# Performance work log

Hardware: AMD Instinct MI355X
Metric: run time of the kernel (lower is better)

The kernel has to match this reference:

```python
import jax, jax.numpy as jnp
import numpy as np


def setup_inputs() -> dict:
    key = jax.random.key(0)
    k1, k2, k3, k4 = jax.random.split(key, 4)
    B, S, D, R = 32, 512, 1024, 256
    batch = jax.random.normal(k1, (B, S, D), dtype=jnp.float32)
    # params initialized uniform(-0.05, 0.05) in the original
    proj_L = jax.random.uniform(k2, (D, R), minval=-0.05, maxval=0.05, dtype=jnp.float32)
    proj_R = jax.random.uniform(k3, (R, D), minval=-0.05, maxval=0.05, dtype=jnp.float32)
    bias = jax.random.uniform(k4, (1,), minval=-0.05, maxval=0.05, dtype=jnp.float32)
    return {"batch": batch, "proj_L": proj_L, "proj_R": proj_R, "bias": bias}


def reference(batch, proj_L, proj_R, bias):
    # logits[b,i,j] = batch[b,i] @ (L @ R) @ batch[b,j] + bias
    # Computed as (batch @ L) @ (batch @ R^T)^T -- two batched GEMMs,
    # avoiding the O(B*S^2*D) expanded intermediate of the original.
    # Dropout is identity in eval mode.
    left = jnp.einsum('bsd,dr->bsr', batch, proj_L)   # [B,S,R]
    right = jnp.einsum('rd,btd->brt', proj_R, batch)  # [B,R,S]
    logits = jnp.einsum('bsr,brt->bst', left, right) + bias[0]
    return logits
```

## Files before the change

### kernel.cpp

```cpp
#include <hip/hip_runtime.h>
#include <hip/hip_bf16.h>
#include <stdint.h>

typedef __attribute__((ext_vector_type(8))) __bf16 bf16x8;
typedef __attribute__((ext_vector_type(4))) float f32x4;

static constexpr int Bb = 32, Ss = 512, Dd = 1024, Rr = 256;

__device__ __forceinline__ void gload_lds16(const void* g, void* l) {
  __builtin_amdgcn_global_load_lds(
      (const __attribute__((address_space(1))) void*)g,
      (__attribute__((address_space(3))) void*)l, 16, 0, 0);
}

__global__ __launch_bounds__(256) void prep_kernel(
    const float* __restrict__ L, const float* __restrict__ R,
    __bf16* __restrict__ Bt) {
  int i = blockIdx.x * 256 + threadIdx.x;
  int n = i >> 10;
  int d = i & (Dd - 1);
  float v = (n < Rr) ? L[d * Rr + n] : R[(size_t)(n - Rr) * Dd + d];
  Bt[i] = (__bf16)v;
}

__global__ __launch_bounds__(256, 4) void proj_gemm(
    const float* __restrict__ batch,
    const __bf16* __restrict__ Bt,
    __bf16* __restrict__ outL,
    __bf16* __restrict__ outR) {
  const int s = (blockIdx.x & 7) * 128 + (blockIdx.x >> 3);
  const int mt = s >> 2;
  const int nt = s & 3;
  const int m0 = mt * 64, n0 = nt * 128;

  __shared__ __align__(16) char smem[32768];

  const int t = threadIdx.x;
  const int lane = t & 63;
  const int wave = t >> 6;
  const int wr = wave >> 1, wc = wave & 1;

  f32x4 acc[2][4] = {};

  for (int it = 0; it < 16; ++it) {
    const int k0 = it * 64;
    __syncthreads();
#pragma unroll
    for (int q = 0; q < 4; ++q) {
      int e = q * 256 + t;
      int row = e >> 4, g = e & 15;
      int gsrc = g ^ (row & 7);
      gload_lds16(batch + (size_t)(m0 + row) * Dd + k0 + gsrc * 4,
                  smem + e * 16);
    }
#pragma unroll
    for (int q = 0; q < 4; ++q) {
      int e = q * 256 + t;
      int row = e >> 3, g = e & 7;
      int gsrc = g ^ (row & 7);
      gload_lds16(Bt + (size_t)(n0 + row) * Dd + k0 + gsrc * 8,
                  smem + 16384 + e * 16);
    }
    __syncthreads();

#pragma unroll
    for (int kk = 0; kk < 2; ++kk) {
      bf16x8 a[2], b[4];
#pragma unroll
      for (int m = 0; m < 2; ++m) {
        int row = wr * 32 + m * 16 + (lane & 15);
        int ga = kk * 8 + (lane >> 4) * 2;
        f32x4 v0 = *(const f32x4*)(smem + row * 256 + ((ga ^ (row & 7))) * 16);
        f32x4 v1 =
            *(const f32x4*)(smem + row * 256 + (((ga + 1) ^ (row & 7))) * 16);
        bf16x8 av;
        av[0] = (__bf16)v0[0]; av[1] = (__bf16)v0[1];
        av[2] = (__bf16)v0[2]; av[3] = (__bf16)v0[3];
        av[4] = (__bf16)v1[0]; av[5] = (__bf16)v1[1];
        av[6] = (__bf16)v1[2]; av[7] = (__bf16)v1[3];
        a[m] = av;
      }
#pragma unroll
      for (int n = 0; n < 4; ++n) {
        int row = wc * 64 + n * 16 + (lane & 15);
        int g = kk * 4 + (lane >> 4);
        b[n] = *(const bf16x8*)(smem + 16384 +
                                (row * 8 + (g ^ (row & 7))) * 16);
      }
#pragma unroll
      for (int m = 0; m < 2; ++m)
#pragma unroll
        for (int n = 0; n < 4; ++n)
          acc[m][n] = __builtin_amdgcn_mfma_f32_16x16x32_bf16(a[m], b[n],
                                                              acc[m][n], 0, 0, 0);
    }
  }

  __bf16* out = (n0 < Rr) ? outL : outR;
  const int cb = n0 & (Rr - 1);
  const int col = lane & 15, rgrp = lane >> 4;
#pragma unroll
  for (int m = 0; m < 2; ++m) {
    int r0 = m0 + wr * 32 + m * 16 + rgrp * 4;
#pragma unroll
    for (int n = 0; n < 4; ++n) {
      int c = cb + wc * 64 + n * 16 + col;
#pragma unroll
      for (int i = 0; i < 4; ++i)
        out[(size_t)(r0 + i) * Rr + c] = (__bf16)acc[m][n][i];
    }
  }
}

__global__ __launch_bounds__(256, 4) void score_gemm(
    const __bf16* __restrict__ left,
    const __bf16* __restrict__ right,
    const float* __restrict__ biasp,
    float* __restrict__ out) {
  const int nt = blockIdx.x;
  const int mt = blockIdx.y;
  const int bz = blockIdx.z;
  const __bf16* A = left + (size_t)bz * Ss * Rr;
  const __bf16* B = right + (size_t)bz * Ss * Rr;
  float* O = out + (size_t)bz * Ss * Ss;
  const int m0 = mt * 64, n0 = nt * 128;

  __shared__ __align__(16) char smem[24576];

  const int t = threadIdx.x;
  const int lane = t & 63;
  const int wave = t >> 6;
  const int wr = wave >> 1, wc = wave & 1;

  f32x4 acc[2][4] = {};

  for (int it = 0; it < 4; ++it) {
    const int k0 = it * 64;
    __syncthreads();
#pragma unroll
    for (int q = 0; q < 2; ++q) {
      int e = q * 256 + t;
      int row = e >> 3, g = e & 7;
      int gsrc = g ^ (row & 7);
      gload_lds16(A + (size_t)(m0 + row) * Rr + k0 + gsrc * 8, smem + e * 16);
    }
#pragma unroll
    for (int q = 0; q < 4; ++q) {
      int e = q * 256 + t;
      int row = e >> 3, g = e & 7;
      int gsrc = g ^ (row & 7);
      gload_lds16(B + (size_t)(n0 + row) * Rr + k0 + gsrc * 8,
                  smem + 8192 + e * 16);
    }
    __syncthreads();

#pragma unroll
    for (int kk = 0; kk < 2; ++kk) {
      bf16x8 a[2], b[4];
#pragma unroll
      for (int m = 0; m < 2; ++m) {
        int row = wr * 32 + m * 16 + (lane & 15);
        int g = kk * 4 + (lane >> 4);
        a[m] = *(const bf16x8*)(smem + (row * 8 + (g ^ (row & 7))) * 16);
      }
#pragma unroll
      for (int n = 0; n < 4; ++n) {
        int row = wc * 64 + n * 16 + (lane & 15);
        int g = kk * 4 + (lane >> 4);
        b[n] = *(const bf16x8*)(smem + 8192 +
                                (row * 8 + (g ^ (row & 7))) * 16);
      }
#pragma unroll
      for (int m = 0; m < 2; ++m)
#pragma unroll
        for (int n = 0; n < 4; ++n)
          acc[m][n] = __builtin_amdgcn_mfma_f32_16x16x32_bf16(a[m], b[n],
                                                              acc[m][n], 0, 0, 0);
    }
  }

  const float bias = *biasp;
  const int col = lane & 15, rgrp = lane >> 4;
#pragma unroll
  for (int m = 0; m < 2; ++m) {
    int r0 = m0 + wr * 32 + m * 16 + rgrp * 4;
#pragma unroll
    for (int n = 0; n < 4; ++n) {
      int c = n0 + wc * 64 + n * 16 + col;
#pragma unroll
      for (int i = 0; i < 4; ++i)
        O[(size_t)(r0 + i) * Ss + c] = acc[m][n][i] + bias;
    }
  }
}

extern "C" void kernel_launch(void* const* d_in, const int* in_sizes, int n_in,
                              void* d_out, int out_size, void* d_ws,
                              size_t ws_size, hipStream_t stream) {
  const float* batch = (const float*)d_in[0];
  const float* projL = (const float*)d_in[1];
  const float* projR = (const float*)d_in[2];
  const float* bias = (const float*)d_in[3];
  float* out = (float*)d_out;

  char* ws = (char*)d_ws;
  __bf16* left = (__bf16*)(ws);
  __bf16* right = (__bf16*)(ws + 8388608);
  __bf16* Btc = (__bf16*)(ws + 16777216);

  prep_kernel<<<dim3(2048), dim3(256), 0, stream>>>(projL, projR, Btc);
  proj_gemm<<<dim3(1024), dim3(256), 0, stream>>>(batch, Btc, left, right);
  score_gemm<<<dim3(4, 8, 32), dim3(256), 0, stream>>>(left, right, bias, out);
}
```

Measured before the change: 52.02 us.

## Rework projection GEMM with larger tiles and double-buffered register-staged prefetch

```diff
diff --git a/kernel.cpp b/kernel.cpp
--- a/kernel.cpp
+++ b/kernel.cpp
@@ -23,88 +23,103 @@
   Bt[i] = (__bf16)v;
 }
 
-__global__ __launch_bounds__(256, 4) void proj_gemm(
+__global__ __launch_bounds__(512, 2) void proj_gemm(
     const float* __restrict__ batch,
     const __bf16* __restrict__ Bt,
     __bf16* __restrict__ outL,
     __bf16* __restrict__ outR) {
-  const int s = (blockIdx.x & 7) * 128 + (blockIdx.x >> 3);
-  const int mt = s >> 2;
-  const int nt = s & 3;
-  const int m0 = mt * 64, n0 = nt * 128;
-
-  __shared__ __align__(16) char smem[32768];
+  const int s = (blockIdx.x & 7) * 32 + (blockIdx.x >> 3);
+  const int mt = s >> 1;
+  const int nt = s & 1;
+  const int m0 = mt * 128, n0 = nt * 256;
+
+  __shared__ __align__(16) char smem[49152];
 
   const int t = threadIdx.x;
   const int lane = t & 63;
   const int wave = t >> 6;
-  const int wr = wave >> 1, wc = wave & 1;
-
-  f32x4 acc[2][4] = {};
-
-  for (int it = 0; it < 16; ++it) {
-    const int k0 = it * 64;
-    __syncthreads();
-#pragma unroll
-    for (int q = 0; q < 4; ++q) {
-      int e = q * 256 + t;
-      int row = e >> 4, g = e & 15;
-      int gsrc = g ^ (row & 7);
-      gload_lds16(batch + (size_t)(m0 + row) * Dd + k0 + gsrc * 4,
-                  smem + e * 16);
-    }
-#pragma unroll
-    for (int q = 0; q < 4; ++q) {
-      int e = q * 256 + t;
-      int row = e >> 3, g = e & 7;
-      int gsrc = g ^ (row & 7);
-      gload_lds16(Bt + (size_t)(n0 + row) * Dd + k0 + gsrc * 8,
-                  smem + 16384 + e * 16);
-    }
-    __syncthreads();
-
-#pragma unroll
-    for (int kk = 0; kk < 2; ++kk) {
-      bf16x8 a[2], b[4];
-#pragma unroll
-      for (int m = 0; m < 2; ++m) {
-        int row = wr * 32 + m * 16 + (lane & 15);
-        int ga = kk * 8 + (lane >> 4) * 2;
-        f32x4 v0 = *(const f32x4*)(smem + row * 256 + ((ga ^ (row & 7))) * 16);
-        f32x4 v1 =
-            *(const f32x4*)(smem + row * 256 + (((ga + 1) ^ (row & 7))) * 16);
-        bf16x8 av;
-        av[0] = (__bf16)v0[0]; av[1] = (__bf16)v0[1];
-        av[2] = (__bf16)v0[2]; av[3] = (__bf16)v0[3];
-        av[4] = (__bf16)v1[0]; av[5] = (__bf16)v1[1];
-        av[6] = (__bf16)v1[2]; av[7] = (__bf16)v1[3];
-        a[m] = av;
-      }
-#pragma unroll
-      for (int n = 0; n < 4; ++n) {
-        int row = wc * 64 + n * 16 + (lane & 15);
-        int g = kk * 4 + (lane >> 4);
-        b[n] = *(const bf16x8*)(smem + 16384 +
-                                (row * 8 + (g ^ (row & 7))) * 16);
-      }
-#pragma unroll
-      for (int m = 0; m < 2; ++m)
-#pragma unroll
-        for (int n = 0; n < 4; ++n)
-          acc[m][n] = __builtin_amdgcn_mfma_f32_16x16x32_bf16(a[m], b[n],
-                                                              acc[m][n], 0, 0, 0);
-    }
-  }
-
-  __bf16* out = (n0 < Rr) ? outL : outR;
-  const int cb = n0 & (Rr - 1);
+  const int wr = wave >> 2, wc = wave & 3;
+
+  f32x4 acc[4][4] = {};
+  f32x4 areg0, areg1;
+
+  const int arow = t >> 2, ag = t & 3;
+  const int ags = ag ^ ((arow >> 1) & 3);
+
+  auto issueA = [&](int k0) {
+    const float* src = batch + (size_t)(m0 + arow) * Dd + k0 + ag * 8;
+    areg0 = *(const f32x4*)src;
+    areg1 = *(const f32x4*)(src + 4);
+  };
+  auto writeA = [&](int buf) {
+    bf16x8 v;
+    v[0] = (__bf16)areg0[0]; v[1] = (__bf16)areg0[1];
+    v[2] = (__bf16)areg0[2]; v[3] = (__bf16)areg0[3];
+    v[4] = (__bf16)areg1[0]; v[5] = (__bf16)areg1[1];
+    v[6] = (__bf16)areg1[2]; v[7] = (__bf16)areg1[3];
+    *(bf16x8*)(smem + buf * 8192 + (arow * 4 + ags) * 16) = v;
+  };
+  auto stageB = [&](int buf, int k0) {
+#pragma unroll
+    for (int p = 0; p < 2; ++p) {
+      int e = p * 512 + t;
+      int row = e >> 2, g = e & 3;
+      int gs = g ^ ((row >> 1) & 3);
+      gload_lds16(Bt + (size_t)(n0 + row) * Dd + k0 + gs * 8,
+                  smem + 16384 + buf * 16384 + e * 16);
+    }
+  };
+  auto compute = [&](int buf) {
+    const char* Ab = smem + buf * 8192;
+    const char* Bb = smem + 16384 + buf * 16384;
+    bf16x8 a[4], b[4];
+    const int g = lane >> 4;
+#pragma unroll
+    for (int m = 0; m < 4; ++m) {
+      int row = wr * 64 + m * 16 + (lane & 15);
+      a[m] = *(const bf16x8*)(Ab + (row * 4 + (g ^ ((row >> 1) & 3))) * 16);
+    }
+#pragma unroll
+    for (int n = 0; n < 4; ++n) {
+      int row = wc * 64 + n * 16 + (lane & 15);
+      b[n] = *(const bf16x8*)(Bb + (row * 4 + (g ^ ((row >> 1) & 3))) * 16);
+    }
+#pragma unroll
+    for (int m = 0; m < 4; ++m)
+#pragma unroll
+      for (int n = 0; n < 4; ++n)
+        acc[m][n] = __builtin_amdgcn_mfma_f32_16x16x32_bf16(a[m], b[n],
+                                                            acc[m][n], 0, 0, 0);
+  };
+
+  issueA(0);
+  stageB(0, 0);
+  writeA(0);
+  int cur = 0;
+  for (int it = 0; it < 32; ++it) {
+    if (it < 31) {
+      issueA(it * 32 + 32);
+      stageB(cur ^ 1, it * 32 + 32);
+      asm volatile("s_waitcnt vmcnt(4)" ::: "memory");
+    } else {
+      asm volatile("s_waitcnt vmcnt(0)" ::: "memory");
+    }
+    __builtin_amdgcn_s_barrier();
+    compute(cur);
+    if (it < 31) writeA(cur ^ 1);
+    asm volatile("s_waitcnt lgkmcnt(0)" ::: "memory");
+    __builtin_amdgcn_s_barrier();
+    cur ^= 1;
+  }
+
+  __bf16* out = nt ? outR : outL;
   const int col = lane & 15, rgrp = lane >> 4;
 #pragma unroll
-  for (int m = 0; m < 2; ++m) {
-    int r0 = m0 + wr * 32 + m * 16 + rgrp * 4;
+  for (int m = 0; m < 4; ++m) {
+    int r0 = m0 + wr * 64 + m * 16 + rgrp * 4;
 #pragma unroll
     for (int n = 0; n < 4; ++n) {
-      int c = cb + wc * 64 + n * 16 + col;
+      int c = wc * 64 + n * 16 + col;
 #pragma unroll
       for (int i = 0; i < 4; ++i)
         out[(size_t)(r0 + i) * Rr + c] = (__bf16)acc[m][n][i];
@@ -209,6 +224,6 @@
   __bf16* Btc = (__bf16*)(ws + 16777216);
 
   prep_kernel<<<dim3(2048), dim3(256), 0, stream>>>(projL, projR, Btc);
-  proj_gemm<<<dim3(1024), dim3(256), 0, stream>>>(batch, Btc, left, right);
+  proj_gemm<<<dim3(256), dim3(512), 0, stream>>>(batch, Btc, left, right);
   score_gemm<<<dim3(4, 8, 32), dim3(256), 0, stream>>>(left, right, bias, out);
 }
```

Measured after the change: 54.28 us. +4.3%, slower.

## Double-buffer proj_gemm and convert batch tile to bf16 once in registers

Applied to the files above, without the earlier changes.

```diff
diff --git a/kernel.cpp b/kernel.cpp
--- a/kernel.cpp
+++ b/kernel.cpp
@@ -23,17 +23,17 @@
   Bt[i] = (__bf16)v;
 }
 
-__global__ __launch_bounds__(256, 4) void proj_gemm(
+__global__ __launch_bounds__(256, 3) void proj_gemm(
     const float* __restrict__ batch,
     const __bf16* __restrict__ Bt,
     __bf16* __restrict__ outL,
     __bf16* __restrict__ outR) {
-  const int s = (blockIdx.x & 7) * 128 + (blockIdx.x >> 3);
+  const int s = ((blockIdx.x & 7) << 7) + (blockIdx.x >> 3);
   const int mt = s >> 2;
   const int nt = s & 3;
   const int m0 = mt * 64, n0 = nt * 128;
 
-  __shared__ __align__(16) char smem[32768];
+  __shared__ __align__(16) char smem[49152];
 
   const int t = threadIdx.x;
   const int lane = t & 63;
@@ -41,51 +41,59 @@
   const int wr = wave >> 1, wc = wave & 1;
 
   f32x4 acc[2][4] = {};
-
-  for (int it = 0; it < 16; ++it) {
-    const int k0 = it * 64;
-    __syncthreads();
-#pragma unroll
-    for (int q = 0; q < 4; ++q) {
-      int e = q * 256 + t;
-      int row = e >> 4, g = e & 15;
-      int gsrc = g ^ (row & 7);
-      gload_lds16(batch + (size_t)(m0 + row) * Dd + k0 + gsrc * 4,
-                  smem + e * 16);
-    }
-#pragma unroll
-    for (int q = 0; q < 4; ++q) {
-      int e = q * 256 + t;
+  f32x4 areg[4];
+
+  const int arow = t >> 2, ag = t & 3;
+  const int ags = ag ^ (arow & 7);
+
+  auto issueA = [&](int k0) {
+    const float* src = batch + (size_t)(m0 + arow) * Dd + k0 + ag * 8;
+    areg[0] = *(const f32x4*)src;
+    areg[1] = *(const f32x4*)(src + 4);
+    areg[2] = *(const f32x4*)(src + 32);
+    areg[3] = *(const f32x4*)(src + 36);
+  };
+  auto writeA = [&](int buf) {
+    char* Ab = smem + buf * 8192;
+    bf16x8 v0, v1;
+    v0[0] = (__bf16)areg[0][0]; v0[1] = (__bf16)areg[0][1];
+    v0[2] = (__bf16)areg[0][2]; v0[3] = (__bf16)areg[0][3];
+    v0[4] = (__bf16)areg[1][0]; v0[5] = (__bf16)areg[1][1];
+    v0[6] = (__bf16)areg[1][2]; v0[7] = (__bf16)areg[1][3];
+    v1[0] = (__bf16)areg[2][0]; v1[1] = (__bf16)areg[2][1];
+    v1[2] = (__bf16)areg[2][2]; v1[3] = (__bf16)areg[2][3];
+    v1[4] = (__bf16)areg[3][0]; v1[5] = (__bf16)areg[3][1];
+    v1[6] = (__bf16)areg[3][2]; v1[7] = (__bf16)areg[3][3];
+    *(bf16x8*)(Ab + (arow * 8 + ags) * 16) = v0;
+    *(bf16x8*)(Ab + (arow * 8 + (ags ^ 4)) * 16) = v1;
+  };
+  auto stageB = [&](int buf, int k0) {
+    char* Bbuf = smem + 16384 + buf * 16384;
+#pragma unroll
+    for (int p = 0; p < 4; ++p) {
+      int e = p * 256 + t;
       int row = e >> 3, g = e & 7;
-      int gsrc = g ^ (row & 7);
-      gload_lds16(Bt + (size_t)(n0 + row) * Dd + k0 + gsrc * 8,
-                  smem + 16384 + e * 16);
-    }
-    __syncthreads();
-
+      int gs = g ^ (row & 7);
+      gload_lds16(Bt + (size_t)(n0 + row) * Dd + k0 + gs * 8,
+                  Bbuf + e * 16);
+    }
+  };
+  auto compute = [&](int buf) {
+    const char* Ab = smem + buf * 8192;
+    const char* Bbuf = smem + 16384 + buf * 16384;
 #pragma unroll
     for (int kk = 0; kk < 2; ++kk) {
+      const int g = kk * 4 + (lane >> 4);
       bf16x8 a[2], b[4];
 #pragma unroll
       for (int m = 0; m < 2; ++m) {
         int row = wr * 32 + m * 16 + (lane & 15);
-        int ga = kk * 8 + (lane >> 4) * 2;
-        f32x4 v0 = *(const f32x4*)(smem + row * 256 + ((ga ^ (row & 7))) * 16);
-        f32x4 v1 =
-            *(const f32x4*)(smem + row * 256 + (((ga + 1) ^ (row & 7))) * 16);
-        bf16x8 av;
-        av[0] = (__bf16)v0[0]; av[1] = (__bf16)v0[1];
-        av[2] = (__bf16)v0[2]; av[3] = (__bf16)v0[3];
-        av[4] = (__bf16)v1[0]; av[5] = (__bf16)v1[1];
-        av[6] = (__bf16)v1[2]; av[7] = (__bf16)v1[3];
-        a[m] = av;
+        a[m] = *(const bf16x8*)(Ab + (row * 8 + (g ^ (row & 7))) * 16);
       }
 #pragma unroll
       for (int n = 0; n < 4; ++n) {
         int row = wc * 64 + n * 16 + (lane & 15);
-        int g = kk * 4 + (lane >> 4);
-        b[n] = *(const bf16x8*)(smem + 16384 +
-                                (row * 8 + (g ^ (row & 7))) * 16);
+        b[n] = *(const bf16x8*)(Bbuf + (row * 8 + (g ^ (row & 7))) * 16);
       }
 #pragma unroll
       for (int m = 0; m < 2; ++m)
@@ -94,6 +102,23 @@
           acc[m][n] = __builtin_amdgcn_mfma_f32_16x16x32_bf16(a[m], b[n],
                                                               acc[m][n], 0, 0, 0);
     }
+  };
+
+  issueA(0);
+  stageB(0, 0);
+  writeA(0);
+  __syncthreads();
+
+#pragma unroll 1
+  for (int tt = 0; tt < 16; ++tt) {
+    const int buf = tt & 1;
+    if (tt < 15) {
+      issueA(tt * 64 + 64);
+      stageB(buf ^ 1, tt * 64 + 64);
+    }
+    compute(buf);
+    if (tt < 15) writeA(buf ^ 1);
+    __syncthreads();
   }
 
   __bf16* out = (n0 < Rr) ? outL : outR;
```

Result: slower. 54.05 us (+3.9%).

## Restructure projection GEMM: direct-register A loads, double-buffered B, 32x32 MFMA

Applied to the files above, without the earlier changes.

```diff
diff --git a/kernel.cpp b/kernel.cpp
--- a/kernel.cpp
+++ b/kernel.cpp
@@ -4,6 +4,7 @@
 
 typedef __attribute__((ext_vector_type(8))) __bf16 bf16x8;
 typedef __attribute__((ext_vector_type(4))) float f32x4;
+typedef __attribute__((ext_vector_type(16))) float f32x16;
 
 static constexpr int Bb = 32, Ss = 512, Dd = 1024, Rr = 256;
 
@@ -23,93 +24,123 @@
   Bt[i] = (__bf16)v;
 }
 
-__global__ __launch_bounds__(256, 4) void proj_gemm(
+__global__ __launch_bounds__(256, 3) void proj_gemm(
     const float* __restrict__ batch,
     const __bf16* __restrict__ Bt,
     __bf16* __restrict__ outL,
     __bf16* __restrict__ outR) {
-  const int s = (blockIdx.x & 7) * 128 + (blockIdx.x >> 3);
+  const int s = ((blockIdx.x & 7) << 6) + (blockIdx.x >> 3);
   const int mt = s >> 2;
   const int nt = s & 3;
-  const int m0 = mt * 64, n0 = nt * 128;
-
-  __shared__ __align__(16) char smem[32768];
+  const int m0 = mt * 128, n0 = nt * 128;
+
+  __shared__ __align__(16) char smem[16384];
 
   const int t = threadIdx.x;
   const int lane = t & 63;
   const int wave = t >> 6;
   const int wr = wave >> 1, wc = wave & 1;
 
-  f32x4 acc[2][4] = {};
-
-  for (int it = 0; it < 16; ++it) {
-    const int k0 = it * 64;
+  f32x16 acc[2][2] = {};
+
+  const float* abase =
+      batch + (size_t)(m0 + wr * 64 + (lane & 31)) * Dd + (lane >> 5) * 8;
+
+  f32x4 anext[8];
+  bf16x8 acur[4];
+
+  auto loadAraw = [&](int k0) {
+#pragma unroll
+    for (int mi = 0; mi < 2; ++mi)
+#pragma unroll
+      for (int ks = 0; ks < 2; ++ks) {
+        const float* p = abase + (size_t)mi * 32 * Dd + k0 + ks * 16;
+        anext[(mi * 2 + ks) * 2] = *(const f32x4*)p;
+        anext[(mi * 2 + ks) * 2 + 1] = *(const f32x4*)(p + 4);
+      }
+  };
+  auto cvtA = [&]() {
+#pragma unroll
+    for (int q = 0; q < 4; ++q) {
+      f32x4 lo = anext[2 * q], hi = anext[2 * q + 1];
+      bf16x8 v;
+      v[0] = (__bf16)lo[0]; v[1] = (__bf16)lo[1];
+      v[2] = (__bf16)lo[2]; v[3] = (__bf16)lo[3];
+      v[4] = (__bf16)hi[0]; v[5] = (__bf16)hi[1];
+      v[6] = (__bf16)hi[2]; v[7] = (__bf16)hi[3];
+      acur[q] = v;
+    }
+  };
+  auto stageB = [&](int buf, int k0) {
+    char* Bbuf = smem + buf * 8192;
+#pragma unroll
+    for (int p = 0; p < 2; ++p) {
+      int e = p * 256 + t;
+      int row = e >> 2, g = e & 3;
+      int gs = g ^ (row & 3);
+      gload_lds16(Bt + (size_t)(n0 + row) * Dd + k0 + gs * 8, Bbuf + e * 16);
+    }
+  };
+
+  loadAraw(0);
+  stageB(0, 0);
+  cvtA();
+  __syncthreads();
+
+#pragma unroll 1
+  for (int tt = 0; tt < 32; ++tt) {
+    const int buf = tt & 1;
+    const char* Bbuf = smem + buf * 8192;
+    if (tt < 31) stageB(buf ^ 1, tt * 32 + 32);
+
+    bf16x8 b0[2], b1[2];
+#pragma unroll
+    for (int ni = 0; ni < 2; ++ni) {
+      int row = wc * 64 + ni * 32 + (lane & 31);
+      int kg = 0 * 2 + (lane >> 5);
+      b0[ni] = *(const bf16x8*)(Bbuf + (row * 4 + (kg ^ (row & 3))) * 16);
+    }
+#pragma unroll
+    for (int mi = 0; mi < 2; ++mi)
+#pragma unroll
+      for (int ni = 0; ni < 2; ++ni)
+        acc[mi][ni] = __builtin_amdgcn_mfma_f32_32x32x16_bf16(
+            acur[mi * 2 + 0], b0[ni], acc[mi][ni], 0, 0, 0);
+
+    if (tt < 31) loadAraw(tt * 32 + 32);
+
+#pragma unroll
+    for (int ni = 0; ni < 2; ++ni) {
+      int row = wc * 64 + ni * 32 + (lane & 31);
+      int kg = 1 * 2 + (lane >> 5);
+      b1[ni] = *(const bf16x8*)(Bbuf + (row * 4 + (kg ^ (row & 3))) * 16);
+    }
+#pragma unroll
+    for (int mi = 0; mi < 2; ++mi)
+#pragma unroll
+      for (int ni = 0; ni < 2; ++ni)
+        acc[mi][ni] = __builtin_amdgcn_mfma_f32_32x32x16_bf16(
+            acur[mi * 2 + 1], b1[ni], acc[mi][ni], 0, 0, 0);
+
     __syncthreads();
-#pragma unroll
-    for (int q = 0; q < 4; ++q) {
-      int e = q * 256 + t;
-      int row = e >> 4, g = e & 15;
-      int gsrc = g ^ (row & 7);
-      gload_lds16(batch + (size_t)(m0 + row) * Dd + k0 + gsrc * 4,
-                  smem + e * 16);
-    }
-#pragma unroll
-    for (int q = 0; q < 4; ++q) {
-      int e = q * 256 + t;
-      int row = e >> 3, g = e & 7;
-      int gsrc = g ^ (row & 7);
-      gload_lds16(Bt + (size_t)(n0 + row) * Dd + k0 + gsrc * 8,
-                  smem + 16384 + e * 16);
-    }
-    __syncthreads();
-
-#pragma unroll
-    for (int kk = 0; kk < 2; ++kk) {
-      bf16x8 a[2], b[4];
-#pragma unroll
-      for (int m = 0; m < 2; ++m) {
-        int row = wr * 32 + m * 16 + (lane & 15);
-        int ga = kk * 8 + (lane >> 4) * 2;
-        f32x4 v0 = *(const f32x4*)(smem + row * 256 + ((ga ^ (row & 7))) * 16);
-        f32x4 v1 =
-            *(const f32x4*)(smem + row * 256 + (((ga + 1) ^ (row & 7))) * 16);
-        bf16x8 av;
-        av[0] = (__bf16)v0[0]; av[1] = (__bf16)v0[1];
-        av[2] = (__bf16)v0[2]; av[3] = (__bf16)v0[3];
-        av[4] = (__bf16)v1[0]; av[5] = (__bf16)v1[1];
-        av[6] = (__bf16)v1[2]; av[7] = (__bf16)v1[3];
-        a[m] = av;
-      }
-#pragma unroll
-      for (int n = 0; n < 4; ++n) {
-        int row = wc * 64 + n * 16 + (lane & 15);
-        int g = kk * 4 + (lane >> 4);
-        b[n] = *(const bf16x8*)(smem + 16384 +
-                                (row * 8 + (g ^ (row & 7))) * 16);
-      }
-#pragma unroll
-      for (int m = 0; m < 2; ++m)
-#pragma unroll
-        for (int n = 0; n < 4; ++n)
-          acc[m][n] = __builtin_amdgcn_mfma_f32_16x16x32_bf16(a[m], b[n],
-                                                              acc[m][n], 0, 0, 0);
-    }
+    if (tt < 31) cvtA();
   }
 
   __bf16* out = (n0 < Rr) ? outL : outR;
   const int cb = n0 & (Rr - 1);
-  const int col = lane & 15, rgrp = lane >> 4;
-#pragma unroll
-  for (int m = 0; m < 2; ++m) {
-    int r0 = m0 + wr * 32 + m * 16 + rgrp * 4;
-#pragma unroll
-    for (int n = 0; n < 4; ++n) {
-      int c = cb + wc * 64 + n * 16 + col;
-#pragma unroll
-      for (int i = 0; i < 4; ++i)
-        out[(size_t)(r0 + i) * Rr + c] = (__bf16)acc[m][n][i];
-    }
-  }
+  const int colb = lane & 31, rowb = 4 * (lane >> 5);
+#pragma unroll
+  for (int mi = 0; mi < 2; ++mi)
+#pragma unroll
+    for (int ni = 0; ni < 2; ++ni) {
+      int rbase = m0 + wr * 64 + mi * 32 + rowb;
+      int c = cb + wc * 64 + ni * 32 + colb;
+#pragma unroll
+      for (int r = 0; r < 16; ++r) {
+        int row = rbase + (r & 3) + 8 * (r >> 2);
+        out[(size_t)row * Rr + c] = (__bf16)acc[mi][ni][r];
+      }
+    }
 }
 
 __global__ __launch_bounds__(256, 4) void score_gemm(
@@ -126,7 +157,6 @@
   const int m0 = mt * 64, n0 = nt * 128;
 
   __shared__ __align__(16) char smem[24576];
-
   const int t = threadIdx.x;
   const int lane = t & 63;
   const int wave = t >> 6;
@@ -209,6 +239,6 @@
   __bf16* Btc = (__bf16*)(ws + 16777216);
 
   prep_kernel<<<dim3(2048), dim3(256), 0, stream>>>(projL, projR, Btc);
-  proj_gemm<<<dim3(1024), dim3(256), 0, stream>>>(batch, Btc, left, right);
+  proj_gemm<<<dim3(512), dim3(256), 0, stream>>>(batch, Btc, left, right);
   score_gemm<<<dim3(4, 8, 32), dim3(256), 0, stream>>>(left, right, bias, out);
 }
```

Result: slower. 91.06 us (+75.0%).
